# Kernel optimization log

Measured on AMD Instinct MI355X. Metric: run time of the kernel, lower is better.

Reference implementation:

```python
import jax, jax.numpy as jnp
import numpy as np

MU = 1.0  # opts.loss_type[1]


def setup_inputs() -> dict:
    key = jax.random.key(0)
    k1, k2 = jax.random.split(key)
    B, D, N = 8, 3, 4096
    srcs = jax.random.normal(k1, (B, D, N), dtype=jnp.float32)
    tgts = jax.random.normal(k2, (B, D, N), dtype=jnp.float32)
    return {"srcs": srcs, "tgts": tgts}


def reference(srcs, tgts):
    # [B, D, N] -> [B, N, D]
    s = jnp.transpose(srcs, (0, 2, 1))
    t = jnp.transpose(tgts, (0, 2, 1))
    # squared euclidean pairwise distances: ||s_i - t_j||^2, [B, N, M]
    s_sq = jnp.sum(s * s, axis=-1)          # [B, N]
    t_sq = jnp.sum(t * t, axis=-1)          # [B, M]
    cross = jnp.einsum('bnd,bmd->bnm', s, t)  # [B, N, M]
    P = s_sq[:, :, None] + t_sq[:, None, :] - 2.0 * cross
    # bidirectional chamfer mins
    d_tgt = jnp.min(P, axis=1)  # min over src points, [B, M]
    d_src = jnp.min(P, axis=2)  # min over tgt points, [B, N]
    distances = jnp.stack([d_tgt, d_src], axis=-1)  # [B, N, 2]
    # Geman-McClure robust penalty
    losses = (MU * distances / (distances + MU)).sum(axis=2).mean(axis=1).mean()
    return losses
```

## Files before the change

kernel.cpp:

```cpp
#include <hip/hip_runtime.h>


#define NPTS 4096
#define NB 8

__global__ __launch_bounds__(1024, 8)
void chamfer_gm_kernel(const float* __restrict__ srcs,
                       const float* __restrict__ tgts,
                       float* __restrict__ out) {
    __shared__ float4 sDB[NPTS];

    const int blk  = blockIdx.x;
    const int pair = blk >> 5;
    const int sub  = blk & 31;
    const int dir  = pair >> 3;
    const int b    = pair & 7;

    const float* qg = (dir == 0 ? srcs : tgts) + b * 3 * NPTS;
    const float* dg = (dir == 0 ? tgts : srcs) + b * 3 * NPTS;

    const int tid = threadIdx.x;

#pragma unroll
    for (int r = 0; r < 4; r++) {
        const int j = tid + r * 1024;
        const float x = dg[j];
        const float y = dg[NPTS + j];
        const float z = dg[2 * NPTS + j];
        sDB[j] = make_float4(-2.0f * x, -2.0f * y, -2.0f * z,
                             fmaf(z, z, fmaf(y, y, x * x)));
    }

    const int wave  = tid >> 6;
    const int lane  = tid & 63;
    const int qbase = sub * 128 + wave * 8;

    float qx[8], qy[8], qz[8], dmin[8];
#pragma unroll
    for (int q = 0; q < 8; q++) {
        qx[q] = qg[qbase + q];
        qy[q] = qg[NPTS + qbase + q];
        qz[q] = qg[2 * NPTS + qbase + q];
        dmin[q] = 3.0e38f;
    }
    __syncthreads();

#pragma unroll 2
    for (int it = 0; it < NPTS / 64; it++) {
        const float4 t = sDB[it * 64 + lane];
#pragma unroll
        for (int q = 0; q < 8; q++) {
            const float v = fmaf(qx[q], t.x,
                           fmaf(qy[q], t.y,
                           fmaf(qz[q], t.z, t.w)));
            dmin[q] = fminf(dmin[q], v);
        }
    }

    float acc = 0.0f;
#pragma unroll
    for (int q = 0; q < 8; q++) {
        float m = dmin[q];
#pragma unroll
        for (int off = 32; off > 0; off >>= 1)
            m = fminf(m, __shfl_xor(m, off, 64));
        const float qs = fmaf(qz[q], qz[q], fmaf(qy[q], qy[q], qx[q] * qx[q]));
        float d = fmaxf(m + qs, 0.0f);
        acc += d / (d + 1.0f);
    }

    __syncthreads();
    float* sPart = (float*)sDB;
    if (lane == 0) sPart[wave] = acc;
    __syncthreads();
    if (tid == 0) {
        float s = 0.0f;
#pragma unroll
        for (int w = 0; w < 16; w++) s += sPart[w];
        atomicAdd(out, s * (1.0f / (NB * NPTS)));
    }
}

extern "C" void kernel_launch(void* const* d_in, const int* in_sizes, int n_in,
                              void* d_out, int out_size, void* d_ws, size_t ws_size,
                              hipStream_t stream) {
    const float* srcs = (const float*)d_in[0];
    const float* tgts = (const float*)d_in[1];
    float* out = (float*)d_out;
    chamfer_gm_kernel<<<dim3(512), dim3(1024), 0, stream>>>(srcs, tgts, out);
}
```

Before: 81.34 us.

## Compute pairwise distances with bf16 MFMA using hi/lo split and partial-min reduction

Replaces the scalar FMA distance loop with MFMA 16x16x32 bf16 matrix ops. Coordinates are split into hi/lo bf16 pairs so the cross term keeps near-fp32 accuracy. Both chamfer directions come from a single pass: row mins are reduced in-kernel, and column mins are written to a large partial buffer that a separate reduce kernel finishes. This halves the distance work and uses matrix cores, but adds four launches, heavy global partial-buffer traffic, and bf16 precision risk.

```diff
diff --git a/kernel.cpp b/kernel.cpp
--- a/kernel.cpp
+++ b/kernel.cpp
@@ -1,83 +1,205 @@
 #include <hip/hip_runtime.h>
 
 
-#define NPTS 4096
-#define NB 8
-
-__global__ __launch_bounds__(1024, 8)
-void chamfer_gm_kernel(const float* __restrict__ srcs,
-                       const float* __restrict__ tgts,
-                       float* __restrict__ out) {
-    __shared__ float4 sDB[NPTS];
-
-    const int blk  = blockIdx.x;
-    const int pair = blk >> 5;
-    const int sub  = blk & 31;
-    const int dir  = pair >> 3;
-    const int b    = pair & 7;
-
-    const float* qg = (dir == 0 ? srcs : tgts) + b * 3 * NPTS;
-    const float* dg = (dir == 0 ? tgts : srcs) + b * 3 * NPTS;
-
-    const int tid = threadIdx.x;
-
-#pragma unroll
-    for (int r = 0; r < 4; r++) {
-        const int j = tid + r * 1024;
-        const float x = dg[j];
-        const float y = dg[NPTS + j];
-        const float z = dg[2 * NPTS + j];
-        sDB[j] = make_float4(-2.0f * x, -2.0f * y, -2.0f * z,
-                             fmaf(z, z, fmaf(y, y, x * x)));
-    }
-
-    const int wave  = tid >> 6;
-    const int lane  = tid & 63;
-    const int qbase = sub * 128 + wave * 8;
-
-    float qx[8], qy[8], qz[8], dmin[8];
-#pragma unroll
-    for (int q = 0; q < 8; q++) {
-        qx[q] = qg[qbase + q];
-        qy[q] = qg[NPTS + qbase + q];
-        qz[q] = qg[2 * NPTS + qbase + q];
-        dmin[q] = 3.0e38f;
+#define NPTS    4096
+#define NB      8
+#define NSTRIPE 128
+#define CTPW    64
+
+typedef __attribute__((ext_vector_type(8))) short bf16x8;
+typedef __attribute__((ext_vector_type(4))) float floatx4;
+
+#define OFF_APACK 0u
+#define OFF_BPACK (1u << 20)
+#define OFF_SSQ   (2u << 20)
+#define OFF_TSQ   ((2u << 20) + (128u << 10))
+#define OFF_PART  ((2u << 20) + (256u << 10))
+#define OFF_ACC   (OFF_PART + (unsigned)(NB * NSTRIPE * NPTS) * 4u)
+
+union V16 { int4 i; bf16x8 h; };
+
+__device__ __forceinline__ unsigned short f2bf(float f) {
+    unsigned u = __float_as_uint(f);
+    u += 0x7FFFu + ((u >> 16) & 1u);
+    return (unsigned short)(u >> 16);
+}
+__device__ __forceinline__ float bf2f(unsigned short h) {
+    return __uint_as_float(((unsigned)h) << 16);
+}
+__device__ __forceinline__ unsigned pk(unsigned short lo, unsigned short hi) {
+    return (unsigned)lo | ((unsigned)hi << 16);
+}
+
+__global__ __launch_bounds__(256)
+void transform_kernel(const float* __restrict__ srcs,
+                      const float* __restrict__ tgts,
+                      char* __restrict__ ws) {
+    const int gid = blockIdx.x * 256 + threadIdx.x;
+    const int b = gid >> 12, j = gid & 4095;
+
+    {
+        const float* sp = srcs + b * 3 * NPTS;
+        const float x = sp[j], y = sp[NPTS + j], z = sp[2 * NPTS + j];
+        const unsigned short hx = f2bf(x), hy = f2bf(y), hz = f2bf(z);
+        const unsigned short lx = f2bf(x - bf2f(hx));
+        const unsigned short ly = f2bf(y - bf2f(hy));
+        const unsigned short lz = f2bf(z - bf2f(hz));
+        const unsigned short a0 = f2bf(-2.0f * bf2f(hx));
+        const unsigned short a1 = f2bf(-2.0f * bf2f(hy));
+        const unsigned short a2 = f2bf(-2.0f * bf2f(hz));
+        const unsigned short l0 = f2bf(-2.0f * bf2f(lx));
+        const unsigned short l1 = f2bf(-2.0f * bf2f(ly));
+        const unsigned short l2 = f2bf(-2.0f * bf2f(lz));
+        int4* Ap = (int4*)(ws + OFF_APACK + (size_t)gid * 32);
+        Ap[0] = make_int4((int)pk(a0, a1), (int)pk(a2, a0),
+                          (int)pk(a1, a2), (int)pk(l0, l1));
+        Ap[1] = make_int4((int)pk(l2, 0), 0, 0, 0);
+        ((float*)(ws + OFF_SSQ))[gid] = fmaf(z, z, fmaf(y, y, x * x));
+    }
+    {
+        const float* tp = tgts + b * 3 * NPTS;
+        const float x = tp[j], y = tp[NPTS + j], z = tp[2 * NPTS + j];
+        const unsigned short hx = f2bf(x), hy = f2bf(y), hz = f2bf(z);
+        const unsigned short lx = f2bf(x - bf2f(hx));
+        const unsigned short ly = f2bf(y - bf2f(hy));
+        const unsigned short lz = f2bf(z - bf2f(hz));
+        int4* Bp = (int4*)(ws + OFF_BPACK + (size_t)gid * 32);
+        Bp[0] = make_int4((int)pk(hx, hy), (int)pk(hz, lx),
+                          (int)pk(ly, lz), (int)pk(hx, hy));
+        Bp[1] = make_int4((int)pk(hz, 0), 0, 0, 0);
+        ((float*)(ws + OFF_TSQ))[gid] = fmaf(z, z, fmaf(y, y, x * x));
+    }
+    if (gid == 0) {
+        float* acc = (float*)(ws + OFF_ACC);
+        acc[0] = 0.0f;
+        acc[1] = 0.0f;
+    }
+}
+
+__global__ __launch_bounds__(256, 4)
+void chamfer_kernel(char* __restrict__ ws) {
+    const int blk    = blockIdx.x;
+    const int b      = blk >> 7;
+    const int stripe = blk & 127;
+    const int wave   = threadIdx.x >> 6;
+    const int lane   = threadIdx.x & 63;
+    const int col16  = lane & 15;
+    const int quad   = lane >> 4;
+
+    const char*  Apack = ws + OFF_APACK;
+    const char*  Bpack = ws + OFF_BPACK;
+    const float* Ssq   = (const float*)(ws + OFF_SSQ);
+    const float* Tsq   = (const float*)(ws + OFF_TSQ);
+    float* part = (float*)(ws + OFF_PART) + (size_t)(b * NSTRIPE + stripe) * NPTS;
+    float* acc  = (float*)(ws + OFF_ACC);
+
+    bf16x8 afrag[2];
+    floatx4 s2[2];
+#pragma unroll
+    for (int rt = 0; rt < 2; rt++) {
+        V16 v; v.i = make_int4(0, 0, 0, 0);
+        if (quad < 2) {
+            const int pt = b * NPTS + stripe * 32 + rt * 16 + col16;
+            v.i = *(const int4*)(Apack + (size_t)pt * 32 + quad * 16);
+        }
+        afrag[rt] = v.h;
+        s2[rt] = *(const floatx4*)(Ssq + b * NPTS + stripe * 32 + rt * 16 + quad * 4);
+    }
+
+    floatx4 smin0, smin1;
+#pragma unroll
+    for (int r = 0; r < 4; r++) { smin0[r] = 3.0e38f; smin1[r] = 3.0e38f; }
+
+    const int ct0 = wave * CTPW;
+    V16 curB; curB.i = make_int4(0, 0, 0, 0);
+    if (quad < 2)
+        curB.i = *(const int4*)(Bpack + (size_t)(b * NPTS + ct0 * 16 + col16) * 32 + quad * 16);
+    float curT = Tsq[b * NPTS + ct0 * 16 + col16];
+
+    for (int i = 0; i < CTPW; i++) {
+        const int ct  = ct0 + i;
+        const int ctn = ct0 + ((i + 1 < CTPW) ? i + 1 : i);
+        V16 nB; nB.i = make_int4(0, 0, 0, 0);
+        if (quad < 2)
+            nB.i = *(const int4*)(Bpack + (size_t)(b * NPTS + ctn * 16 + col16) * 32 + quad * 16);
+        const float nT = Tsq[b * NPTS + ctn * 16 + col16];
+
+        floatx4 c0, c1;
+#pragma unroll
+        for (int r = 0; r < 4; r++) { c0[r] = s2[0][r] + curT; c1[r] = s2[1][r] + curT; }
+        const floatx4 d0 = __builtin_amdgcn_mfma_f32_16x16x32_bf16(afrag[0], curB.h, c0, 0, 0, 0);
+        const floatx4 d1 = __builtin_amdgcn_mfma_f32_16x16x32_bf16(afrag[1], curB.h, c1, 0, 0, 0);
+
+#pragma unroll
+        for (int r = 0; r < 4; r++) {
+            smin0[r] = fminf(smin0[r], d0[r]);
+            smin1[r] = fminf(smin1[r], d1[r]);
+        }
+        float tg = fminf(fminf(fminf(d0[0], d0[1]), fminf(d0[2], d0[3])),
+                         fminf(fminf(d1[0], d1[1]), fminf(d1[2], d1[3])));
+        tg = fminf(tg, __shfl_xor(tg, 16, 64));
+        tg = fminf(tg, __shfl_xor(tg, 32, 64));
+        if (lane < 16) part[ct * 16 + lane] = tg;
+
+        curB = nB; curT = nT;
+    }
+
+#pragma unroll
+    for (int off = 1; off < 16; off <<= 1) {
+#pragma unroll
+        for (int r = 0; r < 4; r++) {
+            smin0[r] = fminf(smin0[r], __shfl_xor(smin0[r], off, 64));
+            smin1[r] = fminf(smin1[r], __shfl_xor(smin1[r], off, 64));
+        }
+    }
+    __shared__ float sSrc[4][32];
+    if (col16 == 0) {
+#pragma unroll
+        for (int r = 0; r < 4; r++) {
+            sSrc[wave][quad * 4 + r]      = smin0[r];
+            sSrc[wave][16 + quad * 4 + r] = smin1[r];
+        }
     }
     __syncthreads();
-
-#pragma unroll 2
-    for (int it = 0; it < NPTS / 64; it++) {
-        const float4 t = sDB[it * 64 + lane];
-#pragma unroll
-        for (int q = 0; q < 8; q++) {
-            const float v = fmaf(qx[q], t.x,
-                           fmaf(qy[q], t.y,
-                           fmaf(qz[q], t.z, t.w)));
-            dmin[q] = fminf(dmin[q], v);
-        }
-    }
-
-    float acc = 0.0f;
-#pragma unroll
-    for (int q = 0; q < 8; q++) {
-        float m = dmin[q];
-#pragma unroll
-        for (int off = 32; off > 0; off >>= 1)
-            m = fminf(m, __shfl_xor(m, off, 64));
-        const float qs = fmaf(qz[q], qz[q], fmaf(qy[q], qy[q], qx[q] * qx[q]));
-        float d = fmaxf(m + qs, 0.0f);
-        acc += d / (d + 1.0f);
-    }
-
+    if (threadIdx.x < 32) {
+        float m = fminf(fminf(sSrc[0][threadIdx.x], sSrc[1][threadIdx.x]),
+                        fminf(sSrc[2][threadIdx.x], sSrc[3][threadIdx.x]));
+        m = fmaxf(m, 0.0f);
+        float g = m / (m + 1.0f);
+#pragma unroll
+        for (int off = 1; off < 32; off <<= 1)
+            g += __shfl_xor(g, off, 64);
+        if (threadIdx.x == 0) atomicAdd(acc + 0, g);
+    }
+}
+
+__global__ __launch_bounds__(256)
+void reduce_tgt_kernel(char* __restrict__ ws) {
+    const int b   = blockIdx.x >> 4;
+    const int col = (blockIdx.x & 15) * 256 + threadIdx.x;
+    const float* part = (const float*)(ws + OFF_PART);
+    float* acc = (float*)(ws + OFF_ACC);
+
+    float m = 3.0e38f;
+    for (int s = 0; s < NSTRIPE; s++)
+        m = fminf(m, part[(size_t)(b * NSTRIPE + s) * NPTS + col]);
+    m = fmaxf(m, 0.0f);
+    float g = m / (m + 1.0f);
+#pragma unroll
+    for (int off = 1; off < 64; off <<= 1)
+        g += __shfl_xor(g, off, 64);
+    __shared__ float sp[4];
+    if ((threadIdx.x & 63) == 0) sp[threadIdx.x >> 6] = g;
     __syncthreads();
-    float* sPart = (float*)sDB;
-    if (lane == 0) sPart[wave] = acc;
-    __syncthreads();
-    if (tid == 0) {
-        float s = 0.0f;
-#pragma unroll
-        for (int w = 0; w < 16; w++) s += sPart[w];
-        atomicAdd(out, s * (1.0f / (NB * NPTS)));
+    if (threadIdx.x == 0)
+        atomicAdd(acc + 1, sp[0] + sp[1] + sp[2] + sp[3]);
+}
+
+__global__ void write_out_kernel(const char* __restrict__ ws,
+                                 float* __restrict__ out) {
+    if (threadIdx.x == 0) {
+        const float* acc = (const float*)(ws + OFF_ACC);
+        out[0] = (acc[0] + acc[1]) * (1.0f / (NB * NPTS));
     }
 }
 
@@ -87,5 +209,10 @@
     const float* srcs = (const float*)d_in[0];
     const float* tgts = (const float*)d_in[1];
     float* out = (float*)d_out;
-    chamfer_gm_kernel<<<dim3(512), dim3(1024), 0, stream>>>(srcs, tgts, out);
-}
+    char* ws = (char*)d_ws;
+
+    transform_kernel<<<dim3(128), dim3(256), 0, stream>>>(srcs, tgts, ws);
+    chamfer_kernel<<<dim3(1024), dim3(256), 0, stream>>>(ws);
+    reduce_tgt_kernel<<<dim3(128), dim3(256), 0, stream>>>(ws);
+    write_out_kernel<<<dim3(1), dim3(64), 0, stream>>>(ws, out);
+}
```

New measurement: 134.3 us. +65.1%, slower.
